# Kernel tuning notes

Measured on AMD Instinct MI355X. Metric: run time of the kernel, lower is better.

Reference implementation:

```python
import jax, jax.numpy as jnp
import numpy as np

NUM_HEAD = 32
NUM_KV_HEAD = 8
HEAD_DIM = 128
EMBED_DIM = 4096
GROUP = NUM_HEAD // NUM_KV_HEAD + 2  # 6: 4 q slots + 1 k + 1 v
TOKENS = 64


def setup_inputs() -> dict:
    key = jax.random.key(0)
    k1, k2, k3 = jax.random.split(key, 3)
    inp = jax.random.normal(k1, (TOKENS, EMBED_DIM), dtype=jnp.float32)
    # fused GQA weight layout from load_parameter: [embed_dim, num_kv_head, group, head_dim]
    weight = jax.random.normal(k2, (EMBED_DIM, NUM_KV_HEAD, GROUP, HEAD_DIM), dtype=jnp.float32) * 0.02
    bias = jax.random.normal(k3, (NUM_KV_HEAD, GROUP, HEAD_DIM), dtype=jnp.float32) * 0.02
    return {"input": inp, "weight": weight, "bias": bias}


def reference(input, weight, bias):
    # fused grouped QKV GEMM (mm_qkv_group_out):
    # out[t, kv, g, d] = sum_e input[t, e] * weight[e, kv, g, d] + bias[kv, g, d]
    out = jnp.einsum('te,ekgd->tkgd', input, weight) + bias
    T = input.shape[0]
    q = out[:, :, : GROUP - 2, :].reshape(T, NUM_HEAD * HEAD_DIM)
    k = out[:, :, GROUP - 2, :].reshape(T, NUM_KV_HEAD * HEAD_DIM)
    v = out[:, :, GROUP - 1, :].reshape(T, NUM_KV_HEAD * HEAD_DIM)
    return (q, k, v)
```

## Files before the change

### kernel.cpp

```cpp
#include <hip/hip_runtime.h>


#define N_COLS 6144
#define K_DIM  4096
#define Q_SZ   (64 * 4096)
#define K_OFF  Q_SZ
#define V_OFF  (Q_SZ + 64 * 1024)
#define OUT_ELEMS 393216
#define NT     48
#define KSPLIT 16
#define BK     32
#define TILES  8

typedef __bf16 bf16x8 __attribute__((ext_vector_type(8)));
typedef float  f32x4  __attribute__((ext_vector_type(4)));

__device__ __forceinline__ int out_index(int t, int n) {
    const int kv = n / 768;
    const int g  = (n >> 7) % 6;
    const int d  = n & 127;
    if (g < 4)  return t * 4096 + kv * 512 + g * 128 + d;
    if (g == 4) return K_OFF + t * 1024 + kv * 128 + d;
    return V_OFF + t * 1024 + kv * 128 + d;
}

__global__ __launch_bounds__(256, 3)
void qkv_gemm(const float* __restrict__ in, const float* __restrict__ w,
              float* __restrict__ part) {
    __shared__ float Ws[2][BK * 128];

    const int tid  = threadIdx.x;
    const int nt   = blockIdx.x % NT;
    const int kq   = blockIdx.x / NT;
    const int n0   = nt * 128;
    const int k0   = kq * (BK * TILES);
    const int wid  = tid >> 6;
    const int lane = tid & 63;
    const int l15  = lane & 15;
    const int kblk = lane >> 4;

    const int t5 = tid >> 5;
    const int c  = tid & 31;

    f32x4 acc[2][4];
    #pragma unroll
    for (int a = 0; a < 2; ++a)
        #pragma unroll
        for (int b = 0; b < 4; ++b) acc[a][b] = (f32x4){0.f, 0.f, 0.f, 0.f};

    f32x4 wreg[2][4];
    float4 alo[4], ahi[4];

    const float* wbase = w + (size_t)k0 * N_COLS + n0 + c * 4;

    auto WLOAD = [&](int s, int set) {
        const float* p = wbase + (size_t)s * BK * N_COLS;
        #pragma unroll
        for (int r = 0; r < 4; ++r)
            wreg[set][r] = *(const f32x4*)(p + (size_t)(r * 8 + t5) * N_COLS);
    };
    auto DSWRITE = [&](int set, int buf) {
        #pragma unroll
        for (int r = 0; r < 4; ++r)
            *(f32x4*)&Ws[buf][(r * 8 + t5) * 128 + 4 * (c ^ (r << 2))] =
                wreg[set][r];
    };
    auto ALOAD = [&](int s) {
        const int kc = k0 + s * BK;
        #pragma unroll
        for (int mi = 0; mi < 4; ++mi) {
            const float* ap = in + (size_t)(mi * 16 + l15) * K_DIM + kc + kblk * 8;
            alo[mi] = *(const float4*)ap;
            ahi[mi] = *(const float4*)(ap + 4);
        }
    };

    WLOAD(0, 0);
    ALOAD(0);
    WLOAD(1, 1);
    DSWRITE(0, 0);
    asm volatile("s_waitcnt lgkmcnt(0)" ::: "memory");
    __builtin_amdgcn_s_barrier();

    #pragma unroll
    for (int s = 0; s < TILES; ++s) {
        bf16x8 av[4];
        #pragma unroll
        for (int mi = 0; mi < 4; ++mi) {
            av[mi][0] = (__bf16)alo[mi].x; av[mi][1] = (__bf16)alo[mi].y;
            av[mi][2] = (__bf16)alo[mi].z; av[mi][3] = (__bf16)alo[mi].w;
            av[mi][4] = (__bf16)ahi[mi].x; av[mi][5] = (__bf16)ahi[mi].y;
            av[mi][6] = (__bf16)ahi[mi].z; av[mi][7] = (__bf16)ahi[mi].w;
        }

        if (s + 2 < TILES) WLOAD(s + 2, s & 1);
        if (s + 1 < TILES) ALOAD(s + 1);

        #pragma unroll
        for (int nfi = 0; nfi < 2; ++nfi) {
            const int nb   = (wid * 2 + nfi) * 16 + l15;
            const int base = kblk * 1024 + (nb ^ (kblk << 4));
            bf16x8 bv;
            #pragma unroll
            for (int j = 0; j < 8; ++j)
                bv[j] = (__bf16)Ws[s & 1][base + j * 128];
            #pragma unroll
            for (int mi = 0; mi < 4; ++mi)
                acc[nfi][mi] = __builtin_amdgcn_mfma_f32_16x16x32_bf16(
                    av[mi], bv, acc[nfi][mi], 0, 0, 0);
        }

        if (s + 1 < TILES) {
            DSWRITE((s + 1) & 1, (s + 1) & 1);
            asm volatile("s_waitcnt lgkmcnt(0)" ::: "memory");
            __builtin_amdgcn_s_barrier();
        }
    }

    float* pb = part + (size_t)kq * OUT_ELEMS;
    #pragma unroll
    for (int nfi = 0; nfi < 2; ++nfi) {
        const int n = n0 + (wid * 2 + nfi) * 16 + l15;
        #pragma unroll
        for (int mi = 0; mi < 4; ++mi) {
            #pragma unroll
            for (int r = 0; r < 4; ++r) {
                const int t = mi * 16 + kblk * 4 + r;
                pb[(size_t)t * N_COLS + n] = acc[nfi][mi][r];
            }
        }
    }
}

__global__ __launch_bounds__(256)
void qkv_reduce(const float* __restrict__ part, const float* __restrict__ bias,
                float* __restrict__ out) {
    const int i = (blockIdx.x * 256 + threadIdx.x) << 2;
    const int t = i / N_COLS;
    const int n = i - t * N_COLS;
    f32x4 s = *(const f32x4*)(bias + n);
    #pragma unroll
    for (int kq = 0; kq < KSPLIT; ++kq)
        s += *(const f32x4*)(part + (size_t)kq * OUT_ELEMS + i);
    *(f32x4*)(out + out_index(t, n)) = s;
}

extern "C" void kernel_launch(void* const* d_in, const int* in_sizes, int n_in,
                              void* d_out, int out_size, void* d_ws, size_t ws_size,
                              hipStream_t stream) {
    const float* in   = (const float*)d_in[0];
    const float* w    = (const float*)d_in[1];
    const float* bias = (const float*)d_in[2];
    float* out  = (float*)d_out;
    float* part = (float*)d_ws;

    qkv_gemm<<<NT * KSPLIT, 256, 0, stream>>>(in, w, part);
    qkv_reduce<<<OUT_ELEMS / 1024, 256, 0, stream>>>(part, bias, out);
}
```

Before: 164.8 us.

## Fuse split-K reduction into GEMM via last-block atomic counter, narrow N tile

Removes the separate reduce kernel. Each N tile keeps an atomic counter, and the last split-K block to finish sums all partials, adds the bias and writes the scattered Q/K/V output. The N tile is halved to 64 columns and split-K reduced from 16 to 8 with twice the K tiles per block. Partials now use a contiguous per-block layout with nontemporal stores. This adds a memset launch, threadfences and a serialized tail reduction done by only 96 blocks, and per-block work shifts toward longer K loops.

```diff
diff --git a/kernel.cpp b/kernel.cpp
--- a/kernel.cpp
+++ b/kernel.cpp
@@ -6,11 +6,11 @@
 #define Q_SZ   (64 * 4096)
 #define K_OFF  Q_SZ
 #define V_OFF  (Q_SZ + 64 * 1024)
-#define OUT_ELEMS 393216
-#define NT     48
-#define KSPLIT 16
+#define NT     96
+#define KSPLIT 8
 #define BK     32
-#define TILES  8
+#define TILES  16
+#define PART_FLOATS (KSPLIT * NT * 4096)
 
 typedef __bf16 bf16x8 __attribute__((ext_vector_type(8)));
 typedef float  f32x4  __attribute__((ext_vector_type(4)));
@@ -26,29 +26,29 @@
 
 __global__ __launch_bounds__(256, 3)
 void qkv_gemm(const float* __restrict__ in, const float* __restrict__ w,
-              float* __restrict__ part) {
-    __shared__ float Ws[2][BK * 128];
+              const float* __restrict__ bias, float* __restrict__ out,
+              float* __restrict__ part, unsigned* __restrict__ cnt) {
+    __shared__ float Ws[2][BK * 64];
+    __shared__ int s_last;
 
     const int tid  = threadIdx.x;
     const int nt   = blockIdx.x % NT;
     const int kq   = blockIdx.x / NT;
-    const int n0   = nt * 128;
+    const int n0   = nt * 64;
     const int k0   = kq * (BK * TILES);
     const int wid  = tid >> 6;
     const int lane = tid & 63;
     const int l15  = lane & 15;
     const int kblk = lane >> 4;
 
-    const int t5 = tid >> 5;
-    const int c  = tid & 31;
+    const int t4 = tid >> 4;
+    const int c  = tid & 15;
 
-    f32x4 acc[2][4];
+    f32x4 acc[4];
     #pragma unroll
-    for (int a = 0; a < 2; ++a)
-        #pragma unroll
-        for (int b = 0; b < 4; ++b) acc[a][b] = (f32x4){0.f, 0.f, 0.f, 0.f};
+    for (int b = 0; b < 4; ++b) acc[b] = (f32x4){0.f, 0.f, 0.f, 0.f};
 
-    f32x4 wreg[2][4];
+    f32x4 wreg[2][2];
     float4 alo[4], ahi[4];
 
     const float* wbase = w + (size_t)k0 * N_COLS + n0 + c * 4;
@@ -56,14 +56,16 @@
     auto WLOAD = [&](int s, int set) {
         const float* p = wbase + (size_t)s * BK * N_COLS;
         #pragma unroll
-        for (int r = 0; r < 4; ++r)
-            wreg[set][r] = *(const f32x4*)(p + (size_t)(r * 8 + t5) * N_COLS);
+        for (int r = 0; r < 2; ++r)
+            wreg[set][r] = *(const f32x4*)(p + (size_t)(r * 16 + t4) * N_COLS);
     };
     auto DSWRITE = [&](int set, int buf) {
         #pragma unroll
-        for (int r = 0; r < 4; ++r)
-            *(f32x4*)&Ws[buf][(r * 8 + t5) * 128 + 4 * (c ^ (r << 2))] =
-                wreg[set][r];
+        for (int r = 0; r < 2; ++r) {
+            const int k  = r * 16 + t4;
+            const int cc = c ^ (((k >> 3) & 3) << 2);
+            *(f32x4*)&Ws[buf][k * 64 + 4 * cc] = wreg[set][r];
+        }
     };
     auto ALOAD = [&](int s) {
         const int kc = k0 + s * BK;
@@ -75,15 +77,7 @@
         }
     };
 
-    WLOAD(0, 0);
-    ALOAD(0);
-    WLOAD(1, 1);
-    DSWRITE(0, 0);
-    asm volatile("s_waitcnt lgkmcnt(0)" ::: "memory");
-    __builtin_amdgcn_s_barrier();
-
-    #pragma unroll
-    for (int s = 0; s < TILES; ++s) {
+    auto STEP = [&](int s, int p) {
         bf16x8 av[4];
         #pragma unroll
         for (int mi = 0; mi < 4; ++mi) {
@@ -92,57 +86,79 @@
             av[mi][4] = (__bf16)ahi[mi].x; av[mi][5] = (__bf16)ahi[mi].y;
             av[mi][6] = (__bf16)ahi[mi].z; av[mi][7] = (__bf16)ahi[mi].w;
         }
-
-        if (s + 2 < TILES) WLOAD(s + 2, s & 1);
+        if (s + 2 < TILES) WLOAD(s + 2, p);
         if (s + 1 < TILES) ALOAD(s + 1);
 
+        const int nb   = wid * 16 + l15;
+        const int base = kblk * 8 * 64 + (nb ^ (kblk << 4));
+        bf16x8 bv;
         #pragma unroll
-        for (int nfi = 0; nfi < 2; ++nfi) {
-            const int nb   = (wid * 2 + nfi) * 16 + l15;
-            const int base = kblk * 1024 + (nb ^ (kblk << 4));
-            bf16x8 bv;
-            #pragma unroll
-            for (int j = 0; j < 8; ++j)
-                bv[j] = (__bf16)Ws[s & 1][base + j * 128];
-            #pragma unroll
-            for (int mi = 0; mi < 4; ++mi)
-                acc[nfi][mi] = __builtin_amdgcn_mfma_f32_16x16x32_bf16(
-                    av[mi], bv, acc[nfi][mi], 0, 0, 0);
-        }
+        for (int j = 0; j < 8; ++j)
+            bv[j] = (__bf16)Ws[p][base + j * 64];
+        #pragma unroll
+        for (int mi = 0; mi < 4; ++mi)
+            acc[mi] = __builtin_amdgcn_mfma_f32_16x16x32_bf16(
+                av[mi], bv, acc[mi], 0, 0, 0);
 
         if (s + 1 < TILES) {
-            DSWRITE((s + 1) & 1, (s + 1) & 1);
+            DSWRITE(p ^ 1, p ^ 1);
             asm volatile("s_waitcnt lgkmcnt(0)" ::: "memory");
             __builtin_amdgcn_s_barrier();
         }
+    };
+
+    WLOAD(0, 0);
+    ALOAD(0);
+    WLOAD(1, 1);
+    DSWRITE(0, 0);
+    asm volatile("s_waitcnt lgkmcnt(0)" ::: "memory");
+    __builtin_amdgcn_s_barrier();
+
+    for (int ss = 0; ss < TILES; ss += 2) {
+        STEP(ss, 0);
+        STEP(ss + 1, 1);
     }
 
-    float* pb = part + (size_t)kq * OUT_ELEMS;
+    float* pb = part + ((size_t)(kq * NT + nt)) * 4096 + wid * 16 + l15;
     #pragma unroll
-    for (int nfi = 0; nfi < 2; ++nfi) {
-        const int n = n0 + (wid * 2 + nfi) * 16 + l15;
+    for (int mi = 0; mi < 4; ++mi) {
         #pragma unroll
-        for (int mi = 0; mi < 4; ++mi) {
-            #pragma unroll
-            for (int r = 0; r < 4; ++r) {
-                const int t = mi * 16 + kblk * 4 + r;
-                pb[(size_t)t * N_COLS + n] = acc[nfi][mi][r];
-            }
+        for (int r = 0; r < 4; ++r) {
+            const int t = mi * 16 + kblk * 4 + r;
+            __builtin_nontemporal_store(acc[mi][r], pb + t * 64);
         }
     }
-}
 
-__global__ __launch_bounds__(256)
-void qkv_reduce(const float* __restrict__ part, const float* __restrict__ bias,
-                float* __restrict__ out) {
-    const int i = (blockIdx.x * 256 + threadIdx.x) << 2;
-    const int t = i / N_COLS;
-    const int n = i - t * N_COLS;
-    f32x4 s = *(const f32x4*)(bias + n);
+    __threadfence();
+    __syncthreads();
+    if (tid == 0) {
+        const unsigned prev = atomicAdd(&cnt[nt], 1u);
+        s_last = (prev == KSPLIT - 1);
+    }
+    __syncthreads();
+    if (!s_last) return;
+    __threadfence();
+
+    f32x4 s4[4];
     #pragma unroll
-    for (int kq = 0; kq < KSPLIT; ++kq)
-        s += *(const f32x4*)(part + (size_t)kq * OUT_ELEMS + i);
-    *(f32x4*)(out + out_index(t, n)) = s;
+    for (int h = 0; h < 4; ++h) {
+        const int v = h * 256 + tid;
+        s4[h] = *(const f32x4*)(bias + n0 + (v & 15) * 4);
+    }
+    #pragma unroll
+    for (int kq2 = 0; kq2 < KSPLIT; ++kq2) {
+        const float* pp = part + ((size_t)(kq2 * NT + nt)) * 4096;
+        #pragma unroll
+        for (int h = 0; h < 4; ++h)
+            s4[h] += *(const f32x4*)(pp + (h * 256 + tid) * 4);
+    }
+    #pragma unroll
+    for (int h = 0; h < 4; ++h) {
+        const int v = h * 256 + tid;
+        const int t = v >> 4;
+        const int n = n0 + (v & 15) * 4;
+        *(f32x4*)(out + out_index(t, n)) = s4[h];
+    }
 }
 
 extern "C" void kernel_launch(void* const* d_in, const int* in_sizes, int n_in,
@@ -153,7 +169,8 @@
     const float* bias = (const float*)d_in[2];
     float* out  = (float*)d_out;
     float* part = (float*)d_ws;
+    unsigned* cnt = (unsigned*)((char*)d_ws + (size_t)PART_FLOATS * 4);
 
-    qkv_gemm<<<NT * KSPLIT, 256, 0, stream>>>(in, w, part);
-    qkv_reduce<<<OUT_ELEMS / 1024, 256, 0, stream>>>(part, bias, out);
+    hipMemsetAsync(cnt, 0, NT * sizeof(unsigned), stream);
+    qkv_gemm<<<NT * KSPLIT, 256, 0, stream>>>(in, w, bias, out, part, cnt);
 }
```

Measured after the change: 282.9 us. 1.72x slower.

## Retile QKV GEMM to narrow N tiles with smaller split-K

Applied to the files above, without the earlier changes.

Changes the GEMM tiling from 128-column tiles with 16-way split-K to 32-column tiles with 4-way split-K and a deeper K step. Each wave now owns a 16-token row block instead of all 64 tokens, and the LDS layout and swizzle are reworked to match. This cuts the partial-sum traffic written and then re-read by the reduce kernel by a factor of four. In exchange, each block reuses its weight tile less across tokens, and the input matrix is fetched more times.

```diff
diff --git a/kernel.cpp b/kernel.cpp
--- a/kernel.cpp
+++ b/kernel.cpp
@@ -7,10 +7,10 @@
 #define K_OFF  Q_SZ
 #define V_OFF  (Q_SZ + 64 * 1024)
 #define OUT_ELEMS 393216
-#define NT     48
-#define KSPLIT 16
-#define BK     32
-#define TILES  8
+#define NT     192
+#define KSPLIT 4
+#define BK     64
+#define TILES  16
 
 typedef __bf16 bf16x8 __attribute__((ext_vector_type(8)));
 typedef float  f32x4  __attribute__((ext_vector_type(4)));
@@ -27,52 +27,51 @@
 __global__ __launch_bounds__(256, 3)
 void qkv_gemm(const float* __restrict__ in, const float* __restrict__ w,
               float* __restrict__ part) {
-    __shared__ float Ws[2][BK * 128];
+    __shared__ float Ws[2][BK * 32];
 
     const int tid  = threadIdx.x;
     const int nt   = blockIdx.x % NT;
     const int kq   = blockIdx.x / NT;
-    const int n0   = nt * 128;
+    const int n0   = nt * 32;
     const int k0   = kq * (BK * TILES);
     const int wid  = tid >> 6;
     const int lane = tid & 63;
     const int l15  = lane & 15;
     const int kblk = lane >> 4;
 
-    const int t5 = tid >> 5;
-    const int c  = tid & 31;
+    const int t3 = tid >> 3;
+    const int c  = tid & 7;
 
-    f32x4 acc[2][4];
-    #pragma unroll
-    for (int a = 0; a < 2; ++a)
-        #pragma unroll
-        for (int b = 0; b < 4; ++b) acc[a][b] = (f32x4){0.f, 0.f, 0.f, 0.f};
+    f32x4 acc[2];
+    acc[0] = (f32x4){0.f, 0.f, 0.f, 0.f};
+    acc[1] = (f32x4){0.f, 0.f, 0.f, 0.f};
 
-    f32x4 wreg[2][4];
-    float4 alo[4], ahi[4];
+    f32x4 wreg[2][2];
+    float4 a[4];
 
     const float* wbase = w + (size_t)k0 * N_COLS + n0 + c * 4;
+    const float* abase = in + (size_t)(wid * 16 + l15) * K_DIM + k0 + kblk * 8;
 
     auto WLOAD = [&](int s, int set) {
         const float* p = wbase + (size_t)s * BK * N_COLS;
         #pragma unroll
-        for (int r = 0; r < 4; ++r)
-            wreg[set][r] = *(const f32x4*)(p + (size_t)(r * 8 + t5) * N_COLS);
+        for (int r = 0; r < 2; ++r)
+            wreg[set][r] = *(const f32x4*)(p + (size_t)(r * 32 + t3) * N_COLS);
     };
     auto DSWRITE = [&](int set, int buf) {
         #pragma unroll
-        for (int r = 0; r < 4; ++r)
-            *(f32x4*)&Ws[buf][(r * 8 + t5) * 128 + 4 * (c ^ (r << 2))] =
-                wreg[set][r];
+        for (int r = 0; r < 2; ++r) {
+            const int k  = r * 32 + t3;
+            const int cc = c ^ (((k >> 3) & 1) << 2);
+            *(f32x4*)&Ws[buf][k * 32 + 4 * cc] = wreg[set][r];
+        }
     };
     auto ALOAD = [&](int s) {
-        const int kc = k0 + s * BK;
-        #pragma unroll
-        for (int mi = 0; mi < 4; ++mi) {
-            const float* ap = in + (size_t)(mi * 16 + l15) * K_DIM + kc + kblk * 8;
-            alo[mi] = *(const float4*)ap;
-            ahi[mi] = *(const float4*)(ap + 4);
-        }
+        const float* ap = abase + (size_t)s * BK;
+        a[0] = *(const float4*)ap;
+        a[1] = *(const float4*)(ap + 4);
+        a[2] = *(const float4*)(ap + 32);
+        a[3] = *(const float4*)(ap + 36);
     };
 
     WLOAD(0, 0);
@@ -84,30 +83,31 @@
 
     #pragma unroll
     for (int s = 0; s < TILES; ++s) {
-        bf16x8 av[4];
+        bf16x8 av[2];
         #pragma unroll
-        for (int mi = 0; mi < 4; ++mi) {
-            av[mi][0] = (__bf16)alo[mi].x; av[mi][1] = (__bf16)alo[mi].y;
-            av[mi][2] = (__bf16)alo[mi].z; av[mi][3] = (__bf16)alo[mi].w;
-            av[mi][4] = (__bf16)ahi[mi].x; av[mi][5] = (__bf16)ahi[mi].y;
-            av[mi][6] = (__bf16)ahi[mi].z; av[mi][7] = (__bf16)ahi[mi].w;
+        for (int h = 0; h < 2; ++h) {
+            av[h][0] = (__bf16)a[2*h].x;   av[h][1] = (__bf16)a[2*h].y;
+            av[h][2] = (__bf16)a[2*h].z;   av[h][3] = (__bf16)a[2*h].w;
+            av[h][4] = (__bf16)a[2*h+1].x; av[h][5] = (__bf16)a[2*h+1].y;
+            av[h][6] = (__bf16)a[2*h+1].z; av[h][7] = (__bf16)a[2*h+1].w;
         }
 
         if (s + 2 < TILES) WLOAD(s + 2, s & 1);
         if (s + 1 < TILES) ALOAD(s + 1);
 
         #pragma unroll
-        for (int nfi = 0; nfi < 2; ++nfi) {
-            const int nb   = (wid * 2 + nfi) * 16 + l15;
-            const int base = kblk * 1024 + (nb ^ (kblk << 4));
-            bf16x8 bv;
+        for (int h = 0; h < 2; ++h) {
             #pragma unroll
-            for (int j = 0; j < 8; ++j)
-                bv[j] = (__bf16)Ws[s & 1][base + j * 128];
-            #pragma unroll
-            for (int mi = 0; mi < 4; ++mi)
-                acc[nfi][mi] = __builtin_amdgcn_mfma_f32_16x16x32_bf16(
-                    av[mi], bv, acc[nfi][mi], 0, 0, 0);
+            for (int nfi = 0; nfi < 2; ++nfi) {
+                const int nb   = nfi * 16 + l15;
+                const int base = (h * 32 + kblk * 8) * 32 + (nb ^ ((kblk & 1) << 4));
+                bf16x8 bv;
+                #pragma unroll
+                for (int j = 0; j < 8; ++j)
+                    bv[j] = (__bf16)Ws[s & 1][base + j * 32];
+                acc[nfi] = __builtin_amdgcn_mfma_f32_16x16x32_bf16(
+                    av[h], bv, acc[nfi], 0, 0, 0);
+            }
         }
 
         if (s + 1 < TILES) {
@@ -120,14 +120,11 @@
     float* pb = part + (size_t)kq * OUT_ELEMS;
     #pragma unroll
     for (int nfi = 0; nfi < 2; ++nfi) {
-        const int n = n0 + (wid * 2 + nfi) * 16 + l15;
+        const int n = n0 + nfi * 16 + l15;
         #pragma unroll
-        for (int mi = 0; mi < 4; ++mi) {
-            #pragma unroll
-            for (int r = 0; r < 4; ++r) {
-                const int t = mi * 16 + kblk * 4 + r;
-                pb[(size_t)t * N_COLS + n] = acc[nfi][mi][r];
-            }
+        for (int r = 0; r < 4; ++r) {
+            const int t = wid * 16 + kblk * 4 + r;
+            pb[(size_t)t * N_COLS + n] = acc[nfi][r];
         }
     }
 }
@@ -135,9 +132,11 @@
 __global__ __launch_bounds__(256)
 void qkv_reduce(const float* __restrict__ part, const float* __restrict__ bias,
                 float* __restrict__ out) {
-    const int i = (blockIdx.x * 256 + threadIdx.x) << 2;
-    const int t = i / N_COLS;
-    const int n = i - t * N_COLS;
+    const int nt = blockIdx.x % NT;
+    const int h  = blockIdx.x / NT;
+    const int t  = h * 32 + (threadIdx.x >> 3);
+    const int n  = nt * 32 + (threadIdx.x & 7) * 4;
+    const size_t i = (size_t)t * N_COLS + n;
     f32x4 s = *(const f32x4*)(bias + n);
     #pragma unroll
     for (int kq = 0; kq < KSPLIT; ++kq)
@@ -155,5 +154,5 @@
     float* part = (float*)d_ws;
 
     qkv_gemm<<<NT * KSPLIT, 256, 0, stream>>>(in, w, part);
-    qkv_reduce<<<OUT_ELEMS / 1024, 256, 0, stream>>>(part, bias, out);
+    qkv_reduce<<<NT * 2, 256, 0, stream>>>(part, bias, out);
 }
```

Result: faster. 161.5 us (-2.0%).
